# Kernel optimization log

Hardware: AMD Instinct MI355X
Metric: run time of the kernel (lower is better)

## Reference

```python
import jax, jax.numpy as jnp
import numpy as np

N = 50000      # nodes
E = 512000     # directed edges (module assumes 2nd half is reverse of 1st half)
DIN = 128      # in_channels
EDIM = 128     # edge_dim (== in_channels, required by HypergraphConv branch)
H = 4          # heads
C = 32         # out_channels per head
EPS = 1e-5     # BatchNorm eps


def _segment_softmax(logits, seg, num):
    # PyG-style scatter softmax over segments (stable: subtract per-segment max)
    m = jax.ops.segment_max(logits, seg, num_segments=num)
    m = jnp.where(jnp.isfinite(m), m, 0.0)
    ex = jnp.exp(logits - m[seg])
    s = jax.ops.segment_sum(ex, seg, num_segments=num)
    return ex / (s[seg] + 1e-16)


def setup_inputs() -> dict:
    key = jax.random.key(0)
    ks = jax.random.split(key, 24)

    def lin(k, fin, fout):
        return (jax.random.normal(k, (fin, fout), jnp.float32) / np.sqrt(fin)).astype(jnp.float32)

    return {
        "x": jax.random.normal(ks[0], (N, DIN), jnp.float32),
        "edge_attr": jax.random.normal(ks[1], (E, EDIM), jnp.float32),
        # TransformerConv params
        "Wq": lin(ks[2], DIN, H * C), "bq": 0.01 * jax.random.normal(ks[3], (H * C,), jnp.float32),
        "Wk": lin(ks[4], DIN, H * C), "bk": 0.01 * jax.random.normal(ks[5], (H * C,), jnp.float32),
        "Wv": lin(ks[6], DIN, H * C), "bv": 0.01 * jax.random.normal(ks[7], (H * C,), jnp.float32),
        "We2": lin(ks[8], EDIM, H * C), "be2": 0.01 * jax.random.normal(ks[9], (H * C,), jnp.float32),
        "We3": lin(ks[10], EDIM, H * C), "be3": 0.01 * jax.random.normal(ks[11], (H * C,), jnp.float32),
        "Wcon": lin(ks[12], H * C, C),
        # BatchNorm1d params
        "bn_w": 1.0 + 0.01 * jax.random.normal(ks[13], (C,), jnp.float32),
        "bn_b": 0.01 * jax.random.normal(ks[14], (C,), jnp.float32),
        # HypergraphConv params (use_attention=False, heads=1)
        "Wh1": lin(ks[15], EDIM, C),
        "Wh2": lin(ks[16], DIN, C),
        "bh": jnp.zeros((C,), jnp.float32),
        # integer inputs
        "edge_index": jax.random.randint(ks[17], (2, E), 0, N, dtype=jnp.int32),
        "batch": jnp.zeros((N,), jnp.int32),
    }


def reference(x, edge_attr, Wq, bq, Wk, bk, Wv, bv, We2, be2, We3, be3, Wcon,
              bn_w, bn_b, Wh1, Wh2, bh, edge_index, batch):
    n = x.shape[0]
    e = edge_index.shape[1]
    src, dst = edge_index[0], edge_index[1]

    # ---- TransformerConv (edge-attention message passing) ----
    q = (x @ Wq + bq).reshape(n, H, C)
    k = (x @ Wk + bk).reshape(n, H, C)
    v = (x @ Wv + bv).reshape(n, H, C)
    ea2 = (edge_attr @ We2 + be2).reshape(e, H, C)
    ea3 = (edge_attr @ We3 + be3).reshape(e, H, C)
    qi, kj, vj = q[dst], k[src], v[src]          # gather per edge: [E,H,C]
    scale = 1.0 / np.sqrt(C)
    a1 = _segment_softmax((qi * kj).sum(-1) * scale, dst, n)    # [E,H]
    a2 = _segment_softmax((qi * ea2).sum(-1) * scale, dst, n)   # [E,H]
    msg = (vj * a1[..., None] + ea3 * a2[..., None]).reshape(e, H * C) @ Wcon  # [E,C]
    x_gat = jax.ops.segment_sum(msg, dst, num_segments=n)       # [N,C]

    # BatchNorm1d (training-mode batch stats, biased var) + exact GELU
    mu = x_gat.mean(0)
    var = ((x_gat - mu) ** 2).mean(0)
    x_gat = jax.nn.gelu(bn_w * (x_gat - mu) * jax.lax.rsqrt(var + EPS) + bn_b,
                        approximate=False)

    # ---- DHT dual hypergraph + HypergraphConv (no attention) ----
    e2 = e // 2
    ei = edge_index[:, :e2]           # first half of (bidirectional) edges
    ea = edge_attr[:e2]
    he_node = jnp.repeat(jnp.arange(e2, dtype=jnp.int32), 2)  # dual-node (edge) ids, [2*E2]
    he_edge = ei.T.reshape(-1)                                 # hyperedge (orig node) ids, [2*E2]

    xh = ea @ Wh1      # lin(edge_attr): [E2,C] (heads=1)
    attr = x @ Wh2     # lin2(x):        [N,C]

    ones = jnp.ones((2 * e2,), jnp.float32)
    deg_d = jax.ops.segment_sum(ones, he_node, num_segments=e2)   # D (== 2 per edge)
    Dinv = jnp.where(deg_d > 0, 1.0 / deg_d, 0.0)
    deg_b = jax.ops.segment_sum(ones, he_edge, num_segments=n)    # B (node degree)
    Binv = jnp.where(deg_b > 0, 1.0 / deg_b, 0.0)

    # propagate 1: dual-node -> hyperedge, norm B, then add hyperedge_attr
    o1 = jax.ops.segment_sum(Binv[he_edge][:, None] * xh[he_node],
                             he_edge, num_segments=n) + attr       # [N,C]
    # propagate 2 (flipped): hyperedge -> dual-node, norm D, add bias
    edge_attr2 = jax.ops.segment_sum(Dinv[he_node][:, None] * o1[he_edge],
                                     he_node, num_segments=e2) + bh  # [E2,C]

    return (x_gat, edge_attr2)
```

## Files before the change

### kernel.cpp

```cpp
#include <hip/hip_runtime.h>
#include <math.h>

#define NN 50000
#define NE 512000
#define NE2 256000
#define SCALE 0.17677669529663687f
#define EPSV 1e-5f

#define OFF_Q      0UL
#define OFF_K      6400000UL
#define OFF_V      12800000UL
#define OFF_ATTR   0UL
#define OFF_O1     1600000UL
#define OFF_XGAT   3200000UL
#define OFF_O1ACC  4800000UL
#define OFF_DEGB   6400000UL
#define OFF_STATS  6450000UL
#define OFF_EX1    19200000UL
#define OFF_EX2    21248000UL
#define OFF_XH     19200000UL
#define OFF_CC2    23296000UL
#define OFF_CC3    56064000UL
#define OFF_SEG    88832000UL
#define OFF_CUR    88883000UL
#define OFF_CNT    88933000UL
#define OFF_INV    88983000UL
#define OFF_SRCS   89495000UL
#define OFF_PART   90007000UL
#define OFF_WBT    90008000UL
#define OFF_BIASB  90024384UL
#define OFF_AGG    90024640UL

typedef __attribute__((ext_vector_type(8))) short bf16x8;
typedef __attribute__((ext_vector_type(8))) unsigned short us8;
typedef __attribute__((ext_vector_type(4))) float f32x4;

__device__ __forceinline__ unsigned short f2bf(float f) {
    unsigned int u = __float_as_uint(f);
    unsigned int r = (u + 0x7FFFu + ((u >> 16) & 1u)) >> 16;
    return (unsigned short)r;
}
__device__ __forceinline__ float bf2f(unsigned short u) {
    return __uint_as_float(((unsigned int)u) << 16);
}

__global__ void pack_w(const float* __restrict__ We2, const float* __restrict__ be2,
                       const float* __restrict__ We3, const float* __restrict__ be3,
                       unsigned short* __restrict__ WbT, float* __restrict__ biasb) {
    const int idx = blockIdx.x * 256 + threadIdx.x;
    if (idx < 32768) {
        const int j = idx >> 7;
        const int k = idx & 127;
        const float w = (j < 128) ? We2[k * 128 + j] : We3[k * 128 + (j - 128)];
        WbT[idx] = f2bf(w);
    } else if (idx < 33024) {
        const int jj = idx - 32768;
        biasb[jj] = (jj < 128) ? be2[jj] : be3[jj - 128];
    }
}

__global__ void k_hist(const int* __restrict__ eidx, int* __restrict__ cnt) {
    const int e = blockIdx.x * 256 + threadIdx.x;
    atomicAdd(&cnt[eidx[NE + e]], 1);
}

__global__ void k_scanA(const int* __restrict__ cnt, int* __restrict__ seg,
                        int* __restrict__ part) {
    __shared__ int sd[256];
    const int tid = threadIdx.x;
    const int i = blockIdx.x * 256 + tid;
    const int v = (i < NN) ? cnt[i] : 0;
    sd[tid] = v;
    __syncthreads();
    for (int off = 1; off < 256; off <<= 1) {
        int t = (tid >= off) ? sd[tid - off] : 0;
        __syncthreads();
        sd[tid] += t;
        __syncthreads();
    }
    if (i < NN) seg[i] = sd[tid] - v;
    if (tid == 255) part[blockIdx.x] = sd[255];
}

__global__ void k_scanB(int* __restrict__ part) {
    __shared__ int sd[256];
    const int tid = threadIdx.x;
    const int v = (tid < 196) ? part[tid] : 0;
    sd[tid] = v;
    __syncthreads();
    for (int off = 1; off < 256; off <<= 1) {
        int t = (tid >= off) ? sd[tid - off] : 0;
        __syncthreads();
        sd[tid] += t;
        __syncthreads();
    }
    if (tid < 196) part[tid] = sd[tid] - v;
}

__global__ void k_scanC(int* __restrict__ seg, const int* __restrict__ part) {
    const int i = blockIdx.x * 256 + threadIdx.x;
    if (i < NN) seg[i] += part[blockIdx.x];
    if (i == 0) seg[NN] = NE;
}

__global__ void k_scatter(const int* __restrict__ eidx, const int* __restrict__ seg,
                          int* __restrict__ cur, int* __restrict__ inv,
                          int* __restrict__ srcs) {
    const int e = blockIdx.x * 256 + threadIdx.x;
    const int dst = eidx[NE + e];
    const int pos = seg[dst] + atomicAdd(&cur[dst], 1);
    inv[e] = pos;
    srcs[pos] = eidx[e];
}

__global__ __launch_bounds__(256)
void gemm_ea(const float* __restrict__ A, const unsigned short* __restrict__ WbT,
             const float* __restrict__ biasb, const int* __restrict__ inv,
             unsigned short* __restrict__ Cc, int half) {
    __shared__ unsigned short As[128 * 72];
    __shared__ unsigned short Bs[128 * 72];
    const int tid = threadIdx.x;
    const int wave = tid >> 6;
    const int lane = tid & 63;
    const int quad = lane >> 4;
    const int l16 = lane & 15;
    const int m0 = (wave & 1) * 64;
    const int n0 = (wave >> 1) * 64;
    const size_t r0 = (size_t)blockIdx.x * 128;

    f32x4 acc[4][4];
    #pragma unroll
    for (int i = 0; i < 4; i++)
        #pragma unroll
        for (int j = 0; j < 4; j++) acc[i][j] = (f32x4){0.f, 0.f, 0.f, 0.f};

    for (int kh = 0; kh < 2; kh++) {
        #pragma unroll
        for (int i = 0; i < 8; i++) {
            const int q = tid + 256 * i;
            const int row = q >> 4;
            const int c4 = q & 15;
            const float4 a4 = *(const float4*)(A + (r0 + row) * 128 + kh * 64 + c4 * 4);
            ushort4 b4;
            b4.x = f2bf(a4.x); b4.y = f2bf(a4.y); b4.z = f2bf(a4.z); b4.w = f2bf(a4.w);
            *(ushort4*)(&As[row * 72 + c4 * 4]) = b4;
        }
        {
            const int n = tid >> 1;
            const int koff = (tid & 1) * 32;
            const unsigned short* src = WbT + (size_t)(half * 128 + n) * 128 + kh * 64 + koff;
            #pragma unroll
            for (int u = 0; u < 4; u++) {
                *(us8*)(&Bs[n * 72 + koff + 8 * u]) = *(const us8*)(src + 8 * u);
            }
        }
        __syncthreads();
        #pragma unroll
        for (int kc = 0; kc < 64; kc += 32) {
            bf16x8 af[4], bf[4];
            #pragma unroll
            for (int i = 0; i < 4; i++)
                af[i] = *(const bf16x8*)(&As[(m0 + 16 * i + l16) * 72 + kc + quad * 8]);
            #pragma unroll
            for (int j = 0; j < 4; j++)
                bf[j] = *(const bf16x8*)(&Bs[(n0 + 16 * j + l16) * 72 + kc + quad * 8]);
            #pragma unroll
            for (int i = 0; i < 4; i++)
                #pragma unroll
                for (int j = 0; j < 4; j++)
                    acc[i][j] = __builtin_amdgcn_mfma_f32_16x16x32_bf16(af[i], bf[j], acc[i][j], 0, 0, 0);
        }
        __syncthreads();
    }
    int posr[16];
    #pragma unroll
    for (int i = 0; i < 4; i++)
        #pragma unroll
        for (int r = 0; r < 4; r++)
            posr[i * 4 + r] = inv[r0 + m0 + 16 * i + quad * 4 + r];
    #pragma unroll
    for (int j = 0; j < 4; j++) {
        const int col = n0 + 16 * j + l16;
        const float bcol = biasb[half * 128 + col];
        #pragma unroll
        for (int i = 0; i < 4; i++) {
            #pragma unroll
            for (int r = 0; r < 4; r++) {
                Cc[(size_t)posr[i * 4 + r] * 128 + col] = f2bf(acc[i][j][r] + bcol);
            }
        }
    }
}

__global__ void qkv_kernel(const float* __restrict__ x,
                           const float* __restrict__ Wq, const float* __restrict__ bq,
                           const float* __restrict__ Wk, const float* __restrict__ bk,
                           const float* __restrict__ Wv, const float* __restrict__ bv,
                           float* __restrict__ q, float* __restrict__ k, float* __restrict__ v) {
    __shared__ float xs[8 * 128];
    const int tid = threadIdx.x;
    const int j = tid & 127;
    const int g = tid >> 7;
    const size_t n0 = (size_t)blockIdx.x * 8;
    ((float4*)xs)[tid] = ((const float4*)(x + n0 * 128))[tid];
    __syncthreads();
    float aq[4] = {0,0,0,0}, ak[4] = {0,0,0,0}, av[4] = {0,0,0,0};
    #pragma unroll 4
    for (int d = 0; d < 128; d++) {
        const float wq = Wq[d*128 + j];
        const float wk = Wk[d*128 + j];
        const float wv = Wv[d*128 + j];
        #pragma unroll
        for (int r = 0; r < 4; r++) {
            const float xv = xs[(g + 2*r)*128 + d];
            aq[r] += xv * wq; ak[r] += xv * wk; av[r] += xv * wv;
        }
    }
    const float bqv = bq[j], bkv = bk[j], bvv = bv[j];
    #pragma unroll
    for (int r = 0; r < 4; r++) {
        const size_t n = n0 + g + 2*r;
        q[n*128 + j] = aq[r] + bqv;
        k[n*128 + j] = ak[r] + bkv;
        v[n*128 + j] = av[r] + bvv;
    }
}

__global__ __launch_bounds__(256)
void attn_pass(const int* __restrict__ seg, const int* __restrict__ srcs,
               const float* __restrict__ q, const float* __restrict__ k,
               const float* __restrict__ v,
               const unsigned short* __restrict__ Cc2, const unsigned short* __restrict__ Cc3,
               float* __restrict__ ex1, float* __restrict__ ex2,
               float* __restrict__ agg) {
    const int lane = threadIdx.x & 63;
    const int d = blockIdx.x * 4 + (threadIdx.x >> 6);
    const int s0 = seg[d], s1 = seg[d + 1];
    const float2 qv = ((const float2*)(q + (size_t)d * 128))[lane];
    const int h = lane >> 4;

    float sh1 = 0.f, sh2 = 0.f;
    for (int i = s0; i < s1; i++) {
        const int src = srcs[i];
        const float2 kv = ((const float2*)(k + (size_t)src * 128))[lane];
        const unsigned int cc = ((const unsigned int*)Cc2)[(size_t)i * 64 + lane];
        float p1 = qv.x * kv.x + qv.y * kv.y;
        float p2 = qv.x * bf2f((unsigned short)(cc & 0xFFFF))
                 + qv.y * bf2f((unsigned short)(cc >> 16));
        #pragma unroll
        for (int off = 8; off > 0; off >>= 1) {
            p1 += __shfl_down(p1, off, 16);
            p2 += __shfl_down(p2, off, 16);
        }
        if ((lane & 15) == 0) {
            const float v1 = __expf(p1 * SCALE);
            const float v2 = __expf(p2 * SCALE);
            ex1[(size_t)i * 4 + h] = v1;
            ex2[(size_t)i * 4 + h] = v2;
            sh1 += v1; sh2 += v2;
        }
    }
    const float r1 = 1.f / (sh1 + 1e-16f);
    const float r2 = 1.f / (sh2 + 1e-16f);
    const float i1 = __shfl(r1, h * 16);
    const float i2 = __shfl(r2, h * 16);

    float ax = 0.f, ay = 0.f;
    for (int i = s0; i < s1; i++) {
        const int src = srcs[i];
        const float2 vv = ((const float2*)(v + (size_t)src * 128))[lane];
        const unsigned int c3 = ((const unsigned int*)Cc3)[(size_t)i * 64 + lane];
        const float a1 = ex1[(size_t)i * 4 + h] * i1;
        const float a2 = ex2[(size_t)i * 4 + h] * i2;
        ax += a1 * vv.x + a2 * bf2f((unsigned short)(c3 & 0xFFFF));
        ay += a1 * vv.y + a2 * bf2f((unsigned short)(c3 >> 16));
    }
    ((float2*)(agg + (size_t)d * 128))[lane] = (float2){ax, ay};
}

__global__ void gemm_d128_o32(const float* __restrict__ A, const float* __restrict__ W,
                              float* __restrict__ out) {
    __shared__ float as[8 * 128];
    const int tid = threadIdx.x;
    const int p = tid & 31;
    const int mm = tid >> 5;
    const size_t m0 = (size_t)blockIdx.x * 8;
    ((float4*)as)[tid] = ((const float4*)(A + m0 * 128))[tid];
    __syncthreads();
    float c0 = 0.f, c1 = 0.f, c2 = 0.f, c3 = 0.f;
    const float4* as4 = (const float4*)as;
    #pragma unroll 8
    for (int i = 0; i < 32; i++) {
        const float4 a4 = as4[mm*32 + i];
        c0 += a4.x * W[(4*i+0)*32 + p];
        c1 += a4.y * W[(4*i+1)*32 + p];
        c2 += a4.z * W[(4*i+2)*32 + p];
        c3 += a4.w * W[(4*i+3)*32 + p];
    }
    out[(m0 + mm)*32 + p] = (c0 + c1) + (c2 + c3);
}

__global__ void bn_stats(const float* __restrict__ xg, float* __restrict__ stats) {
    __shared__ float ls[256], lss[256];
    const int tid = threadIdx.x;
    float s = 0.f, ss = 0.f;
    for (size_t i = (size_t)blockIdx.x*256 + tid; i < (size_t)NN*32; i += (size_t)gridDim.x*256) {
        const float val = xg[i];
        s += val; ss += val * val;
    }
    ls[tid] = s; lss[tid] = ss;
    __syncthreads();
    if (tid < 32) {
        float as_ = 0.f, ass = 0.f;
        #pragma unroll
        for (int w = 0; w < 8; w++) { as_ += ls[tid + 32*w]; ass += lss[tid + 32*w]; }
        atomicAdd(&stats[tid], as_);
        atomicAdd(&stats[32 + tid], ass);
    }
}

__global__ void bn_gelu(const float* __restrict__ xg, const float* __restrict__ stats,
                        const float* __restrict__ bnw, const float* __restrict__ bnb,
                        float* __restrict__ out) {
    const size_t i = (size_t)blockIdx.x * 256 + threadIdx.x;
    const int c = i & 31;
    const float mu = stats[c] * (1.0f / NN);
    const float var = stats[32 + c] * (1.0f / NN) - mu * mu;
    const float xn = bnw[c] * (xg[i] - mu) * rsqrtf(var + EPSV) + bnb[c];
    out[i] = 0.5f * xn * (1.0f + erff(xn * 0.70710678118654752f));
}

__global__ void hyper_scatter(const float* __restrict__ xh, const int* __restrict__ eidx,
                              float* __restrict__ o1acc, float* __restrict__ degb) {
    const int tid = threadIdx.x;
    const int c = tid & 31;
    const size_t i = (size_t)blockIdx.x * 8 + (tid >> 5);
    const int src = eidx[i];
    const int dst = eidx[NE + i];
    const float xv = xh[i*32 + c];
    atomicAdd(&o1acc[(size_t)src*32 + c], xv);
    atomicAdd(&o1acc[(size_t)dst*32 + c], xv);
    if (c == 0) {
        atomicAdd(&degb[src], 1.0f);
        atomicAdd(&degb[dst], 1.0f);
    }
}

__global__ void o1_finalize(const float* __restrict__ o1acc, const float* __restrict__ degb,
                            const float* __restrict__ attr, float* __restrict__ o1) {
    const size_t i = (size_t)blockIdx.x * 256 + threadIdx.x;
    const int n = (int)(i >> 5);
    const float d = degb[n];
    const float binv = d > 0.f ? 1.0f / d : 0.0f;
    o1[i] = o1acc[i] * binv + attr[i];
}

__global__ void edge_out(const float* __restrict__ o1, const int* __restrict__ eidx,
                         const float* __restrict__ bh, float* __restrict__ out2) {
    const size_t idx = (size_t)blockIdx.x * 256 + threadIdx.x;
    const size_t i = idx >> 5;
    const int c = (int)(idx & 31);
    const int src = eidx[i];
    const int dst = eidx[NE + i];
    out2[idx] = 0.5f * (o1[(size_t)src*32 + c] + o1[(size_t)dst*32 + c]) + bh[c];
}

extern "C" void kernel_launch(void* const* d_in, const int* in_sizes, int n_in,
                              void* d_out, int out_size, void* d_ws, size_t ws_size,
                              hipStream_t stream) {
    const float* x    = (const float*)d_in[0];
    const float* eatt = (const float*)d_in[1];
    const float* Wq   = (const float*)d_in[2];
    const float* bq   = (const float*)d_in[3];
    const float* Wk   = (const float*)d_in[4];
    const float* bk   = (const float*)d_in[5];
    const float* Wv   = (const float*)d_in[6];
    const float* bv   = (const float*)d_in[7];
    const float* We2  = (const float*)d_in[8];
    const float* be2  = (const float*)d_in[9];
    const float* We3  = (const float*)d_in[10];
    const float* be3  = (const float*)d_in[11];
    const float* Wcon = (const float*)d_in[12];
    const float* bnw  = (const float*)d_in[13];
    const float* bnb  = (const float*)d_in[14];
    const float* Wh1  = (const float*)d_in[15];
    const float* Wh2  = (const float*)d_in[16];
    const float* bh   = (const float*)d_in[17];
    const int*   eidx = (const int*)d_in[18];

    float* ws = (float*)d_ws;
    float* q     = ws + OFF_Q;
    float* k     = ws + OFF_K;
    float* v     = ws + OFF_V;
    float* ex1   = ws + OFF_EX1;
    float* ex2   = ws + OFF_EX2;
    unsigned short* Cc2 = (unsigned short*)(ws + OFF_CC2);
    unsigned short* Cc3 = (unsigned short*)(ws + OFF_CC3);
    int* seg  = (int*)(ws + OFF_SEG);
    int* cur  = (int*)(ws + OFF_CUR);
    int* cnt  = (int*)(ws + OFF_CNT);
    int* inv  = (int*)(ws + OFF_INV);
    int* srcs = (int*)(ws + OFF_SRCS);
    int* part = (int*)(ws + OFF_PART);
    unsigned short* WbT = (unsigned short*)(ws + OFF_WBT);
    float* biasb = ws + OFF_BIASB;
    float* agg   = ws + OFF_AGG;
    float* attr  = ws + OFF_ATTR;
    float* o1    = ws + OFF_O1;
    float* xgat  = ws + OFF_XGAT;
    float* o1acc = ws + OFF_O1ACC;
    float* degb  = ws + OFF_DEGB;
    float* stats = ws + OFF_STATS;
    float* xh    = ws + OFF_XH;
    float* out0  = (float*)d_out;
    float* out1  = (float*)d_out + (size_t)NN * 32;

    hipMemsetAsync(ws + OFF_CUR, 0, 100000 * sizeof(int), stream);

    pack_w<<<129, 256, 0, stream>>>(We2, be2, We3, be3, WbT, biasb);

    k_hist<<<2000, 256, 0, stream>>>(eidx, cnt);
    k_scanA<<<196, 256, 0, stream>>>(cnt, seg, part);
    k_scanB<<<1, 256, 0, stream>>>(part);
    k_scanC<<<196, 256, 0, stream>>>(seg, part);
    k_scatter<<<2000, 256, 0, stream>>>(eidx, seg, cur, inv, srcs);

    qkv_kernel<<<6250, 256, 0, stream>>>(x, Wq, bq, Wk, bk, Wv, bv, q, k, v);

    gemm_ea<<<4000, 256, 0, stream>>>(eatt, WbT, biasb, inv, Cc2, 0);
    gemm_ea<<<4000, 256, 0, stream>>>(eatt, WbT, biasb, inv, Cc3, 1);

    attn_pass<<<12500, 256, 0, stream>>>(seg, srcs, q, k, v, Cc2, Cc3, ex1, ex2, agg);

    hipMemsetAsync(ws + OFF_O1ACC, 0, (6450064UL - OFF_O1ACC) * sizeof(float), stream);

    gemm_d128_o32<<<6250, 256, 0, stream>>>(agg, Wcon, xgat);
    bn_stats<<<256, 256, 0, stream>>>(xgat, stats);
    bn_gelu<<<6250, 256, 0, stream>>>(xgat, stats, bnw, bnb, out0);

    gemm_d128_o32<<<32000, 256, 0, stream>>>(eatt, Wh1, xh);
    gemm_d128_o32<<<6250, 256, 0, stream>>>(x, Wh2, attr);
    hyper_scatter<<<32000, 256, 0, stream>>>(xh, eidx, o1acc, degb);
    o1_finalize<<<6250, 256, 0, stream>>>(o1acc, degb, attr, o1);
    edge_out<<<32000, 256, 0, stream>>>(o1, eidx, bh, out1);
}
```

Measured before the change: 1.180 ms.

## Fuse edge GEMMs into one launch and single-pass attention with prefetch

Merges the two edge-attribute GEMM launches into one kernel that computes both 128-column halves per block, so edge_attr is read and converted to bf16 once instead of twice. The attention kernel becomes a single pass with online accumulation: it skips the max-subtraction (as the old code already did), accumulates the exp-weighted values directly, and normalizes at the end. This drops the ex1/ex2 scratch writes and the second gather over k/v/Cc. A one-step software prefetch of the next neighbor's rows is added. The cost is higher register pressure: 32 accumulators per wave in the GEMM, plus the prefetch registers in the attention loop.

```diff
diff --git a/kernel.cpp b/kernel.cpp
--- a/kernel.cpp
+++ b/kernel.cpp
@@ -16,8 +16,6 @@
 #define OFF_O1ACC  4800000UL
 #define OFF_DEGB   6400000UL
 #define OFF_STATS  6450000UL
-#define OFF_EX1    19200000UL
-#define OFF_EX2    21248000UL
 #define OFF_XH     19200000UL
 #define OFF_CC2    23296000UL
 #define OFF_CC3    56064000UL
@@ -114,64 +112,64 @@
 }
 
 __global__ __launch_bounds__(256)
-void gemm_ea(const float* __restrict__ A, const unsigned short* __restrict__ WbT,
-             const float* __restrict__ biasb, const int* __restrict__ inv,
-             unsigned short* __restrict__ Cc, int half) {
+void gemm_ea2(const float* __restrict__ A, const unsigned short* __restrict__ WbT,
+              const float* __restrict__ biasb, const int* __restrict__ inv,
+              unsigned short* __restrict__ Cc2, unsigned short* __restrict__ Cc3) {
     __shared__ unsigned short As[128 * 72];
-    __shared__ unsigned short Bs[128 * 72];
+    __shared__ unsigned short Bs[256 * 72];
     const int tid = threadIdx.x;
     const int wave = tid >> 6;
     const int lane = tid & 63;
     const int quad = lane >> 4;
     const int l16 = lane & 15;
     const int m0 = (wave & 1) * 64;
-    const int n0 = (wave >> 1) * 64;
+    const int half = wave >> 1;
+    const int n0g = half * 128;
     const size_t r0 = (size_t)blockIdx.x * 128;
 
-    f32x4 acc[4][4];
+    f32x4 acc[4][8];
     #pragma unroll
     for (int i = 0; i < 4; i++)
         #pragma unroll
-        for (int j = 0; j < 4; j++) acc[i][j] = (f32x4){0.f, 0.f, 0.f, 0.f};
+        for (int j = 0; j < 8; j++) acc[i][j] = (f32x4){0.f, 0.f, 0.f, 0.f};
 
     for (int kh = 0; kh < 2; kh++) {
         #pragma unroll
         for (int i = 0; i < 8; i++) {
-            const int q = tid + 256 * i;
-            const int row = q >> 4;
-            const int c4 = q & 15;
+            const int qq = tid + 256 * i;
+            const int row = qq >> 4;
+            const int c4 = qq & 15;
             const float4 a4 = *(const float4*)(A + (r0 + row) * 128 + kh * 64 + c4 * 4);
             ushort4 b4;
             b4.x = f2bf(a4.x); b4.y = f2bf(a4.y); b4.z = f2bf(a4.z); b4.w = f2bf(a4.w);
             *(ushort4*)(&As[row * 72 + c4 * 4]) = b4;
         }
         {
-            const int n = tid >> 1;
-            const int koff = (tid & 1) * 32;
-            const unsigned short* src = WbT + (size_t)(half * 128 + n) * 128 + kh * 64 + koff;
+            const unsigned short* src = WbT + (size_t)tid * 128 + kh * 64;
             #pragma unroll
-            for (int u = 0; u < 4; u++) {
-                *(us8*)(&Bs[n * 72 + koff + 8 * u]) = *(const us8*)(src + 8 * u);
+            for (int u = 0; u < 8; u++) {
+                *(us8*)(&Bs[tid * 72 + 8 * u]) = *(const us8*)(src + 8 * u);
             }
         }
         __syncthreads();
         #pragma unroll
         for (int kc = 0; kc < 64; kc += 32) {
-            bf16x8 af[4], bf[4];
+            bf16x8 af[4], bf[8];
             #pragma unroll
             for (int i = 0; i < 4; i++)
                 af[i] = *(const bf16x8*)(&As[(m0 + 16 * i + l16) * 72 + kc + quad * 8]);
             #pragma unroll
-            for (int j = 0; j < 4; j++)
-                bf[j] = *(const bf16x8*)(&Bs[(n0 + 16 * j + l16) * 72 + kc + quad * 8]);
+            for (int j = 0; j < 8; j++)
+                bf[j] = *(const bf16x8*)(&Bs[(n0g + 16 * j + l16) * 72 + kc + quad * 8]);
             #pragma unroll
             for (int i = 0; i < 4; i++)
                 #pragma unroll
-                for (int j = 0; j < 4; j++)
+                for (int j = 0; j < 8; j++)
                     acc[i][j] = __builtin_amdgcn_mfma_f32_16x16x32_bf16(af[i], bf[j], acc[i][j], 0, 0, 0);
         }
         __syncthreads();
     }
+    unsigned short* __restrict__ Cc = half ? Cc3 : Cc2;
     int posr[16];
     #pragma unroll
     for (int i = 0; i < 4; i++)
@@ -179,9 +177,9 @@
         for (int r = 0; r < 4; r++)
             posr[i * 4 + r] = inv[r0 + m0 + 16 * i + quad * 4 + r];
     #pragma unroll
-    for (int j = 0; j < 4; j++) {
-        const int col = n0 + 16 * j + l16;
-        const float bcol = biasb[half * 128 + col];
+    for (int j = 0; j < 8; j++) {
+        const int col = 16 * j + l16;
+        const float bcol = biasb[n0g + col];
         #pragma unroll
         for (int i = 0; i < 4; i++) {
             #pragma unroll
@@ -231,51 +229,55 @@
                const float* __restrict__ q, const float* __restrict__ k,
                const float* __restrict__ v,
                const unsigned short* __restrict__ Cc2, const unsigned short* __restrict__ Cc3,
-               float* __restrict__ ex1, float* __restrict__ ex2,
                float* __restrict__ agg) {
     const int lane = threadIdx.x & 63;
     const int d = blockIdx.x * 4 + (threadIdx.x >> 6);
-    const int s0 = seg[d], s1 = seg[d + 1];
+    const int s0 = seg[d], s1e = seg[d + 1];
     const float2 qv = ((const float2*)(q + (size_t)d * 128))[lane];
-    const int h = lane >> 4;
-
+
+    float axv = 0.f, ayv = 0.f;
+    float axe = 0.f, aye = 0.f;
     float sh1 = 0.f, sh2 = 0.f;
-    for (int i = s0; i < s1; i++) {
-        const int src = srcs[i];
-        const float2 kv = ((const float2*)(k + (size_t)src * 128))[lane];
-        const unsigned int cc = ((const unsigned int*)Cc2)[(size_t)i * 64 + lane];
-        float p1 = qv.x * kv.x + qv.y * kv.y;
-        float p2 = qv.x * bf2f((unsigned short)(cc & 0xFFFF))
-                 + qv.y * bf2f((unsigned short)(cc >> 16));
+
+    float2 kv_c = {0.f, 0.f}, vv_c = {0.f, 0.f};
+    unsigned int cc_c = 0, c3_c = 0;
+    if (s0 < s1e) {
+        const int sc = srcs[s0];
+        kv_c = ((const float2*)(k + (size_t)sc * 128))[lane];
+        vv_c = ((const float2*)(v + (size_t)sc * 128))[lane];
+        cc_c = ((const unsigned int*)Cc2)[(size_t)s0 * 64 + lane];
+        c3_c = ((const unsigned int*)Cc3)[(size_t)s0 * 64 + lane];
+    }
+    for (int i = s0; i < s1e; i++) {
+        float2 kv_n = {0.f, 0.f}, vv_n = {0.f, 0.f};
+        unsigned int cc_n = 0, c3_n = 0;
+        if (i + 1 < s1e) {
+            const int sn = srcs[i + 1];
+            kv_n = ((const float2*)(k + (size_t)sn * 128))[lane];
+            vv_n = ((const float2*)(v + (size_t)sn * 128))[lane];
+            cc_n = ((const unsigned int*)Cc2)[(size_t)(i + 1) * 64 + lane];
+            c3_n = ((const unsigned int*)Cc3)[(size_t)(i + 1) * 64 + lane];
+        }
+        float p1 = qv.x * kv_c.x + qv.y * kv_c.y;
+        float p2 = qv.x * bf2f((unsigned short)(cc_c & 0xFFFF))
+                 + qv.y * bf2f((unsigned short)(cc_c >> 16));
         #pragma unroll
         for (int off = 8; off > 0; off >>= 1) {
-            p1 += __shfl_down(p1, off, 16);
-            p2 += __shfl_down(p2, off, 16);
-        }
-        if ((lane & 15) == 0) {
-            const float v1 = __expf(p1 * SCALE);
-            const float v2 = __expf(p2 * SCALE);
-            ex1[(size_t)i * 4 + h] = v1;
-            ex2[(size_t)i * 4 + h] = v2;
-            sh1 += v1; sh2 += v2;
-        }
+            p1 += __shfl_xor(p1, off, 16);
+            p2 += __shfl_xor(p2, off, 16);
+        }
+        const float e1 = __expf(p1 * SCALE);
+        const float e2 = __expf(p2 * SCALE);
+        sh1 += e1; sh2 += e2;
+        axv += e1 * vv_c.x;  ayv += e1 * vv_c.y;
+        axe += e2 * bf2f((unsigned short)(c3_c & 0xFFFF));
+        aye += e2 * bf2f((unsigned short)(c3_c >> 16));
+        kv_c = kv_n; vv_c = vv_n; cc_c = cc_n; c3_c = c3_n;
     }
     const float r1 = 1.f / (sh1 + 1e-16f);
     const float r2 = 1.f / (sh2 + 1e-16f);
-    const float i1 = __shfl(r1, h * 16);
-    const float i2 = __shfl(r2, h * 16);
-
-    float ax = 0.f, ay = 0.f;
-    for (int i = s0; i < s1; i++) {
-        const int src = srcs[i];
-        const float2 vv = ((const float2*)(v + (size_t)src * 128))[lane];
-        const unsigned int c3 = ((const unsigned int*)Cc3)[(size_t)i * 64 + lane];
-        const float a1 = ex1[(size_t)i * 4 + h] * i1;
-        const float a2 = ex2[(size_t)i * 4 + h] * i2;
-        ax += a1 * vv.x + a2 * bf2f((unsigned short)(c3 & 0xFFFF));
-        ay += a1 * vv.y + a2 * bf2f((unsigned short)(c3 >> 16));
-    }
-    ((float2*)(agg + (size_t)d * 128))[lane] = (float2){ax, ay};
+    ((float2*)(agg + (size_t)d * 128))[lane] = (float2){axv * r1 + axe * r2,
+                                                        ayv * r1 + aye * r2};
 }
 
 __global__ void gemm_d128_o32(const float* __restrict__ A, const float* __restrict__ W,
@@ -392,8 +394,6 @@
     float* q     = ws + OFF_Q;
     float* k     = ws + OFF_K;
     float* v     = ws + OFF_V;
-    float* ex1   = ws + OFF_EX1;
-    float* ex2   = ws + OFF_EX2;
     unsigned short* Cc2 = (unsigned short*)(ws + OFF_CC2);
     unsigned short* Cc3 = (unsigned short*)(ws + OFF_CC3);
     int* seg  = (int*)(ws + OFF_SEG);
@@ -427,10 +427,9 @@
 
     qkv_kernel<<<6250, 256, 0, stream>>>(x, Wq, bq, Wk, bk, Wv, bv, q, k, v);
 
-    gemm_ea<<<4000, 256, 0, stream>>>(eatt, WbT, biasb, inv, Cc2, 0);
-    gemm_ea<<<4000, 256, 0, stream>>>(eatt, WbT, biasb, inv, Cc3, 1);
-
-    attn_pass<<<12500, 256, 0, stream>>>(seg, srcs, q, k, v, Cc2, Cc3, ex1, ex2, agg);
+    gemm_ea2<<<4000, 256, 0, stream>>>(eatt, WbT, biasb, inv, Cc2, Cc3);
+
+    attn_pass<<<12500, 256, 0, stream>>>(seg, srcs, q, k, v, Cc2, Cc3, agg);
 
     hipMemsetAsync(ws + OFF_O1ACC, 0, (6450064UL - OFF_O1ACC) * sizeof(float), stream);
 
```

Measured after the change: 1.069 ms. 9.4% less time.
